# Kernel optimization log

Hardware: AMD Instinct MI355X
Metric: run time of the kernel (lower is better)

The kernel has to match this reference:

```python
import jax, jax.numpy as jnp
import numpy as np

IN_FEATURES = 4096
OUT_FEATURES = 12288
INT8_MAX = 127.0


def setup_inputs() -> dict:
    key = jax.random.key(0)
    kx, kw, ks, kb = jax.random.split(key, 4)
    x = jax.random.normal(kx, (8192, IN_FEATURES), dtype=jnp.float32)
    # pre-quantized int8 weight, stored [out_features, in_features] like the torch module
    weight = jax.random.randint(kw, (OUT_FEATURES, IN_FEATURES), -127, 128, dtype=jnp.int8)
    # per-output-channel weight scale, [out_features, 1]
    weight_scale = (jax.random.uniform(ks, (OUT_FEATURES, 1), dtype=jnp.float32) * 0.02 + 1e-4)
    bias = jax.random.normal(kb, (OUT_FEATURES,), dtype=jnp.float32) * 0.01
    return {"x": x, "weight": weight, "weight_scale": weight_scale, "bias": bias}


def _dynamic_int8_quant(x):
    # symmetric per-token quantization: scale = amax(|x|) / 127
    amax = jnp.max(jnp.abs(x), axis=-1, keepdims=True)  # [M, 1]
    scale = jnp.maximum(amax, 1e-8) / INT8_MAX
    x_q = jnp.clip(jnp.round(x / scale), -INT8_MAX, INT8_MAX).astype(jnp.int8)
    return x_q, scale


def reference(x, weight, weight_scale, bias):
    x_q, x_scale = _dynamic_int8_quant(x)                    # [M,K] int8, [M,1] f32
    # int8 GEMM with int32 accumulation: [M,K] @ [K,N]
    acc = jnp.matmul(x_q.astype(jnp.int32), weight.T.astype(jnp.int32))  # [M,N] int32
    # epilogue: dequant with per-token and per-channel scales, then bias add
    out = acc.astype(jnp.float32) * x_scale * weight_scale[:, 0][None, :] + bias[None, :]
    return out.astype(x.dtype)
```

## Files before the change

### kernel.cpp

```cpp
#include <hip/hip_runtime.h>
#include <stdint.h>

#define M_DIM 8192
#define K_DIM 4096
#define N_DIM 12288

typedef int v4i __attribute__((ext_vector_type(4)));

#define GLDS16(g, l)                                                         \
  __builtin_amdgcn_global_load_lds(                                          \
      (const __attribute__((address_space(1))) void*)(g),                    \
      (__attribute__((address_space(3))) void*)(l), 16, 0, 0)

#define BARRIER() asm volatile("s_barrier" ::: "memory")
#define VMCNT2() asm volatile("s_waitcnt vmcnt(2)" ::: "memory")
#define VMCNT0() asm volatile("s_waitcnt vmcnt(0)" ::: "memory")

__global__ __launch_bounds__(256) void prep(const float* __restrict__ x,
                                            int8_t* __restrict__ xq,
                                            float* __restrict__ xs,
                                            const int* __restrict__ w32,
                                            int8_t* __restrict__ w8) {
  const int t = threadIdx.x;
  if ((int)blockIdx.x < M_DIM) {
    const int row = blockIdx.x;
    const float* xr = x + (size_t)row * K_DIM;

    float4 v[4];
    float amax = 0.f;
#pragma unroll
    for (int i = 0; i < 4; ++i) {
      v[i] = reinterpret_cast<const float4*>(xr)[t * 4 + i];
      amax = fmaxf(amax, fmaxf(fmaxf(fabsf(v[i].x), fabsf(v[i].y)),
                               fmaxf(fabsf(v[i].z), fabsf(v[i].w))));
    }
#pragma unroll
    for (int off = 32; off > 0; off >>= 1)
      amax = fmaxf(amax, __shfl_xor(amax, off));

    __shared__ float smax[4];
    if ((t & 63) == 0) smax[t >> 6] = amax;
    __syncthreads();
    amax = fmaxf(fmaxf(smax[0], smax[1]), fmaxf(smax[2], smax[3]));

    const float scale = fmaxf(amax, 1e-8f) / 127.f;

    union {
      int8_t b[16];
      v4i v;
    } p;
    const float* pv = reinterpret_cast<const float*>(v);
#pragma unroll
    for (int i = 0; i < 16; ++i) {
      float r = rintf(pv[i] / scale);
      r = fminf(127.f, fmaxf(-127.f, r));
      p.b[i] = (int8_t)(int)r;
    }
    reinterpret_cast<v4i*>(xq + (size_t)row * K_DIM)[t] = p.v;
    if (t == 0) xs[row] = scale;
  } else {
    const size_t i = (((size_t)blockIdx.x - M_DIM) * 256 + t) * 16;
    const int4* src = reinterpret_cast<const int4*>(w32 + i);
    union {
      int8_t b[16];
      v4i v;
    } p;
#pragma unroll
    for (int c = 0; c < 4; ++c) {
      int4 q = src[c];
      p.b[c * 4 + 0] = (int8_t)q.x;
      p.b[c * 4 + 1] = (int8_t)q.y;
      p.b[c * 4 + 2] = (int8_t)q.z;
      p.b[c * 4 + 3] = (int8_t)q.w;
    }
    *reinterpret_cast<v4i*>(w8 + i) = p.v;
  }
}

#define BM 256
#define BN 256
#define BKB 128
#define NTILES (K_DIM / BKB)

__global__ __launch_bounds__(512, 2) void gemm_i8(
    const int8_t* __restrict__ xq, const float* __restrict__ xs,
    const int8_t* __restrict__ w8, const float* __restrict__ wsc,
    const float* __restrict__ bias, float* __restrict__ out) {
  __shared__ __align__(16) int8_t lds[131072];

  const int t = threadIdx.x;
  const int lane = t & 63;
  const int w = t >> 6;
  const int wr = w >> 2;
  const int wc = w & 3;
  const int fr = lane & 15;
  const int kq = lane >> 4;
  const int l7 = lane & 7;

  {
  }
  const int bid = (int)blockIdx.x;
  const int xcd = bid & 7;
  const int q = bid >> 3;
  const int g = q >> 5;
  const int j = q & 31;
  const int rowBase = (xcd * 4 + (j >> 3)) * BM;
  const int colBase = (g * 8 + (j & 7)) * BN;

  const int srow = t >> 3;
  const int gslot = (t & 7) ^ (srow & 7);
  const int8_t* gA = xq + (size_t)(rowBase + srow) * K_DIM + gslot * 16;
  const int8_t* gB = w8 + (size_t)(colBase + srow) * K_DIM + gslot * 16;
  int8_t* ldsw = lds + w * 1024;

#define STAGE_A(c, r0, k0) \
  GLDS16(gA + (size_t)(r0) * K_DIM + (k0), ldsw + (c) * 32768 + (r0) * 128)
#define STAGE_B(c, r0, k0) \
  GLDS16(gB + (size_t)(r0) * K_DIM + (k0), ldsw + 65536 + (c) * 32768 + (r0) * 128)

  const int s0_ = kq ^ l7;
  const int s1_ = s0_ ^ 4;
  const int rA = wr * 128 + fr;
  const int rB = wc * 64 + fr;

  const v4i* pA0 = (const v4i*)lds + ((rA << 3) + s0_);
  const v4i* pA1 = (const v4i*)lds + ((rA << 3) + s1_);
  const v4i* pB0 = (const v4i*)(lds + 65536) + ((rB << 3) + s0_);
  const v4i* pB1 = (const v4i*)(lds + 65536) + ((rB << 3) + s1_);

  v4i acc[8][4];
#pragma unroll
  for (int i = 0; i < 8; ++i)
#pragma unroll
    for (int jj = 0; jj < 4; ++jj) acc[i][jj] = (v4i){0, 0, 0, 0};

  STAGE_B(0, 0, 0); STAGE_B(0, 64, 0); STAGE_B(0, 128, 0); STAGE_B(0, 192, 0);
  STAGE_A(0, 0, 0); STAGE_A(0, 128, 0); STAGE_A(0, 64, 0); STAGE_A(0, 192, 0);
  VMCNT2();
  BARRIER();

  v4i af[4], bf[4];

#define PHASE(c, MH, KS, LOADB, STG, WAIT)                                    \
  {                                                                           \
    const v4i* _pa = (KS) ? pA1 : pA0;                                        \
    af[0] = _pa[((c) << 11) + (((MH)*64 + 0) << 3)];                          \
    af[1] = _pa[((c) << 11) + (((MH)*64 + 16) << 3)];                         \
    af[2] = _pa[((c) << 11) + (((MH)*64 + 32) << 3)];                         \
    af[3] = _pa[((c) << 11) + (((MH)*64 + 48) << 3)];                         \
    if (LOADB) {                                                              \
      const v4i* _pb = (KS) ? pB1 : pB0;                                      \
      bf[0] = _pb[((c) << 11) + (0 << 3)];                                    \
      bf[1] = _pb[((c) << 11) + (16 << 3)];                                   \
      bf[2] = _pb[((c) << 11) + (32 << 3)];                                   \
      bf[3] = _pb[((c) << 11) + (48 << 3)];                                   \
    }                                                                         \
    STG;                                                                      \
    BARRIER();                                                                \
    __builtin_amdgcn_s_setprio(1);                                            \
    _Pragma("unroll") for (int ni = 0; ni < 4; ++ni)                          \
        _Pragma("unroll") for (int mi = 0; mi < 4; ++mi)                      \
            acc[(MH) * 4 + mi][ni] = __builtin_amdgcn_mfma_i32_16x16x64_i8(   \
                af[mi], bf[ni], acc[(MH) * 4 + mi][ni], 0, 0, 0);             \
    __builtin_amdgcn_s_setprio(0);                                            \
    WAIT;                                                                     \
    BARRIER();                                                                \
  }

#define TILE(c, d, k1)                                                        \
  PHASE(c, 0, 0, 1, { STAGE_B(d, 0, k1); STAGE_B(d, 64, k1); }, VMCNT2());    \
  PHASE(c, 1, 0, 0, { STAGE_B(d, 128, k1); STAGE_B(d, 192, k1); }, );         \
  PHASE(c, 0, 1, 1, { STAGE_A(d, 0, k1); STAGE_A(d, 128, k1); }, );           \
  PHASE(c, 1, 1, 0, { STAGE_A(d, 64, k1); STAGE_A(d, 192, k1); }, VMCNT2());

  for (int tt = 0; tt < NTILES - 2; tt += 2) {
    const int k1a = (tt + 1) * BKB;
    const int k1b = (tt + 2) * BKB;
    TILE(0, 1, k1a);
    TILE(1, 0, k1b);
  }
  TILE(0, 1, (NTILES - 1) * BKB);
  {
    PHASE(1, 0, 0, 1, , VMCNT0());
    PHASE(1, 1, 0, 0, , );
    PHASE(1, 0, 1, 1, , );
    PHASE(1, 1, 1, 0, , );
  }

  const int orow0 = rowBase + wr * 128;
  const int ocol0 = colBase + wc * 64;
  const int rsub = kq * 4;
#pragma unroll
  for (int mi8 = 0; mi8 < 8; ++mi8) {
    const int r0 = orow0 + mi8 * 16 + rsub;
    float s4[4];
#pragma unroll
    for (int r = 0; r < 4; ++r) s4[r] = xs[r0 + r];
#pragma unroll
    for (int ni = 0; ni < 4; ++ni) {
      const int col = ocol0 + ni * 16 + fr;
      const float wf = wsc[col];
      const float bb = bias[col];
#pragma unroll
      for (int r = 0; r < 4; ++r)
        out[(size_t)(r0 + r) * N_DIM + col] =
            (float)acc[mi8][ni][r] * s4[r] * wf + bb;
    }
  }
}

extern "C" void kernel_launch(void* const* d_in, const int* in_sizes, int n_in,
                              void* d_out, int out_size, void* d_ws,
                              size_t ws_size, hipStream_t stream) {
  const float* x = (const float*)d_in[0];
  const int* w32 = (const int*)d_in[1];
  const float* wscale = (const float*)d_in[2];
  const float* bias = (const float*)d_in[3];
  float* out = (float*)d_out;

  int8_t* xq = (int8_t*)d_ws;
  float* xs = (float*)((char*)d_ws + (size_t)M_DIM * K_DIM);
  int8_t* w8 = (int8_t*)((char*)d_ws + (size_t)M_DIM * K_DIM + M_DIM * 4);

  const int packBlocks = (N_DIM * K_DIM) / (256 * 16);
  prep<<<M_DIM + packBlocks, 256, 0, stream>>>(x, xq, xs, w32, w8);
  gemm_i8<<<(M_DIM / BM) * (N_DIM / BN), 512, 0, stream>>>(xq, xs, w8, wscale,
                                                           bias, out);
}
```

Baseline: 461.2 us.

## Restructure int8 GEMM main loop with register double-buffered fragments and one barrier per tile

Replaces the four-phase-per-tile schedule, which had two barriers per phase, with a loop that issues all eight global-to-LDS copies for the next tile up front. LDS fragment reads are double-buffered in registers (a0/a1, b0/b1), so each MFMA block overlaps with the next fragment loads. There is a single vmcnt(0) wait and barrier per K tile. This is meant to cut barrier stalls and expose more overlap of LDS reads with MFMA. In exchange it needs more VGPRs for the extra fragments and waits on all outstanding loads once per tile.

```diff
diff --git a/kernel.cpp b/kernel.cpp
--- a/kernel.cpp
+++ b/kernel.cpp
@@ -13,7 +13,6 @@
       (__attribute__((address_space(3))) void*)(l), 16, 0, 0)
 
 #define BARRIER() asm volatile("s_barrier" ::: "memory")
-#define VMCNT2() asm volatile("s_waitcnt vmcnt(2)" ::: "memory")
 #define VMCNT0() asm volatile("s_waitcnt vmcnt(0)" ::: "memory")
 
 __global__ __launch_bounds__(256) void prep(const float* __restrict__ x,
@@ -97,8 +96,6 @@
   const int kq = lane >> 4;
   const int l7 = lane & 7;
 
-  {
-  }
   const int bid = (int)blockIdx.x;
   const int xcd = bid & 7;
   const int q = bid >> 3;
@@ -118,6 +115,12 @@
 #define STAGE_B(c, r0, k0) \
   GLDS16(gB + (size_t)(r0) * K_DIM + (k0), ldsw + 65536 + (c) * 32768 + (r0) * 128)
 
+#define STAGE8(d, k1)                                                         \
+  STAGE_B(d, 0, k1); STAGE_B(d, 64, k1);                                      \
+  STAGE_B(d, 128, k1); STAGE_B(d, 192, k1);                                   \
+  STAGE_A(d, 0, k1); STAGE_A(d, 64, k1);                                      \
+  STAGE_A(d, 128, k1); STAGE_A(d, 192, k1);
+
   const int s0_ = kq ^ l7;
   const int s1_ = s0_ ^ 4;
   const int rA = wr * 128 + fr;
@@ -128,64 +131,76 @@
   const v4i* pB0 = (const v4i*)(lds + 65536) + ((rB << 3) + s0_);
   const v4i* pB1 = (const v4i*)(lds + 65536) + ((rB << 3) + s1_);
 
+#define LDA(dst, c, mh, ks)                                                   \
+  {                                                                           \
+    const v4i* _p = (ks) ? pA1 : pA0;                                         \
+    dst[0] = _p[((c) << 11) + (((mh) * 64 + 0) << 3)];                        \
+    dst[1] = _p[((c) << 11) + (((mh) * 64 + 16) << 3)];                       \
+    dst[2] = _p[((c) << 11) + (((mh) * 64 + 32) << 3)];                       \
+    dst[3] = _p[((c) << 11) + (((mh) * 64 + 48) << 3)];                       \
+  }
+#define LDB(dst, c, ks)                                                       \
+  {                                                                           \
+    const v4i* _p = (ks) ? pB1 : pB0;                                         \
+    dst[0] = _p[((c) << 11) + (0 << 3)];                                      \
+    dst[1] = _p[((c) << 11) + (16 << 3)];                                     \
+    dst[2] = _p[((c) << 11) + (32 << 3)];                                     \
+    dst[3] = _p[((c) << 11) + (48 << 3)];                                     \
+  }
+
+#define MFMA_BLK(MH, A_, B_)                                                  \
+  __builtin_amdgcn_s_setprio(1);                                              \
+  _Pragma("unroll") for (int ni = 0; ni < 4; ++ni)                            \
+      _Pragma("unroll") for (int mi = 0; mi < 4; ++mi)                        \
+          acc[(MH) * 4 + mi][ni] = __builtin_amdgcn_mfma_i32_16x16x64_i8(     \
+              A_[mi], B_[ni], acc[(MH) * 4 + mi][ni], 0, 0, 0);               \
+  __builtin_amdgcn_s_setprio(0);
+
   v4i acc[8][4];
 #pragma unroll
   for (int i = 0; i < 8; ++i)
 #pragma unroll
     for (int jj = 0; jj < 4; ++jj) acc[i][jj] = (v4i){0, 0, 0, 0};
 
-  STAGE_B(0, 0, 0); STAGE_B(0, 64, 0); STAGE_B(0, 128, 0); STAGE_B(0, 192, 0);
-  STAGE_A(0, 0, 0); STAGE_A(0, 128, 0); STAGE_A(0, 64, 0); STAGE_A(0, 192, 0);
-  VMCNT2();
+  v4i a0[4], a1[4], b0[4], b1[4];
+
+#define TILE(c, d, k1)                                                        \
+  STAGE8(d, k1);                                                              \
+  LDA(a1, c, 1, 0);                                                           \
+  MFMA_BLK(0, a0, b0);                                                        \
+  LDA(a0, c, 0, 1);                                                           \
+  LDB(b1, c, 1);                                                              \
+  MFMA_BLK(1, a1, b0);                                                        \
+  LDA(a1, c, 1, 1);                                                           \
+  MFMA_BLK(0, a0, b1);                                                        \
+  MFMA_BLK(1, a1, b1);                                                        \
+  VMCNT0();                                                                   \
+  BARRIER();                                                                  \
+  LDA(a0, d, 0, 0);                                                           \
+  LDB(b0, d, 0);
+
+#define TILE_LAST(c)                                                          \
+  LDA(a1, c, 1, 0);                                                           \
+  MFMA_BLK(0, a0, b0);                                                        \
+  LDA(a0, c, 0, 1);                                                           \
+  LDB(b1, c, 1);                                                              \
+  MFMA_BLK(1, a1, b0);                                                        \
+  LDA(a1, c, 1, 1);                                                           \
+  MFMA_BLK(0, a0, b1);                                                        \
+  MFMA_BLK(1, a1, b1);
+
+  STAGE8(0, 0);
+  VMCNT0();
   BARRIER();
-
-  v4i af[4], bf[4];
-
-#define PHASE(c, MH, KS, LOADB, STG, WAIT)                                    \
-  {                                                                           \
-    const v4i* _pa = (KS) ? pA1 : pA0;                                        \
-    af[0] = _pa[((c) << 11) + (((MH)*64 + 0) << 3)];                          \
-    af[1] = _pa[((c) << 11) + (((MH)*64 + 16) << 3)];                         \
-    af[2] = _pa[((c) << 11) + (((MH)*64 + 32) << 3)];                         \
-    af[3] = _pa[((c) << 11) + (((MH)*64 + 48) << 3)];                         \
-    if (LOADB) {                                                              \
-      const v4i* _pb = (KS) ? pB1 : pB0;                                      \
-      bf[0] = _pb[((c) << 11) + (0 << 3)];                                    \
-      bf[1] = _pb[((c) << 11) + (16 << 3)];                                   \
-      bf[2] = _pb[((c) << 11) + (32 << 3)];                                   \
-      bf[3] = _pb[((c) << 11) + (48 << 3)];                                   \
-    }                                                                         \
-    STG;                                                                      \
-    BARRIER();                                                                \
-    __builtin_amdgcn_s_setprio(1);                                            \
-    _Pragma("unroll") for (int ni = 0; ni < 4; ++ni)                          \
-        _Pragma("unroll") for (int mi = 0; mi < 4; ++mi)                      \
-            acc[(MH) * 4 + mi][ni] = __builtin_amdgcn_mfma_i32_16x16x64_i8(   \
-                af[mi], bf[ni], acc[(MH) * 4 + mi][ni], 0, 0, 0);             \
-    __builtin_amdgcn_s_setprio(0);                                            \
-    WAIT;                                                                     \
-    BARRIER();                                                                \
-  }
-
-#define TILE(c, d, k1)                                                        \
-  PHASE(c, 0, 0, 1, { STAGE_B(d, 0, k1); STAGE_B(d, 64, k1); }, VMCNT2());    \
-  PHASE(c, 1, 0, 0, { STAGE_B(d, 128, k1); STAGE_B(d, 192, k1); }, );         \
-  PHASE(c, 0, 1, 1, { STAGE_A(d, 0, k1); STAGE_A(d, 128, k1); }, );           \
-  PHASE(c, 1, 1, 0, { STAGE_A(d, 64, k1); STAGE_A(d, 192, k1); }, VMCNT2());
+  LDA(a0, 0, 0, 0);
+  LDB(b0, 0, 0);
 
   for (int tt = 0; tt < NTILES - 2; tt += 2) {
-    const int k1a = (tt + 1) * BKB;
-    const int k1b = (tt + 2) * BKB;
-    TILE(0, 1, k1a);
-    TILE(1, 0, k1b);
+    TILE(0, 1, (tt + 1) * BKB);
+    TILE(1, 0, (tt + 2) * BKB);
   }
   TILE(0, 1, (NTILES - 1) * BKB);
-  {
-    PHASE(1, 0, 0, 1, , VMCNT0());
-    PHASE(1, 1, 0, 0, , );
-    PHASE(1, 0, 1, 1, , );
-    PHASE(1, 1, 1, 0, , );
-  }
+  TILE_LAST(1);
 
   const int orow0 = rowBase + wr * 128;
   const int ocol0 = colBase + wc * 64;
```

Result: no change. 465.4 us (+0.9%).
